# Kernel optimization log

Hardware: AMD Instinct MI355X
Metric: run time of the kernel (lower is better)

The kernel has to match this reference:

```python
import jax, jax.numpy as jnp
import numpy as np

N_NODES = 500_000
N_EDGES = 8_000_000
IN_DIM, HID_DIM, OUT_DIM = 10, 35, 2


def setup_inputs() -> dict:
    key = jax.random.key(0)
    k1, k2, k3, k4 = jax.random.split(key, 4)
    x = jax.random.normal(k1, (N_NODES, IN_DIM), dtype=jnp.float32)
    edge_index = jax.random.randint(k2, (2, N_EDGES), 0, N_NODES, dtype=jnp.int64)
    # Glorot-style init for GCNConv weights
    W1 = jax.random.normal(k3, (IN_DIM, HID_DIM), dtype=jnp.float32) * (1.0 / np.sqrt(IN_DIM))
    b1 = jnp.zeros((HID_DIM,), dtype=jnp.float32)
    W2 = jax.random.normal(k4, (HID_DIM, OUT_DIM), dtype=jnp.float32) * (1.0 / np.sqrt(HID_DIM))
    b2 = jnp.zeros((OUT_DIM,), dtype=jnp.float32)
    return {"x": x, "edge_index": edge_index, "W1": W1, "b1": b1, "W2": W2, "b2": b2}


def reference(x, edge_index, W1, b1, W2, b2):
    N = x.shape[0]
    # GCNConv: add self-loops, symmetric normalization D^-1/2 (A+I) D^-1/2
    loops = jnp.arange(N, dtype=edge_index.dtype)
    src = jnp.concatenate([edge_index[0], loops])  # [E+N]
    dst = jnp.concatenate([edge_index[1], loops])  # [E+N]
    deg = jax.ops.segment_sum(jnp.ones(src.shape, dtype=x.dtype), dst, num_segments=N)
    dinv = jax.lax.rsqrt(jnp.maximum(deg, 1.0))  # deg >= 1 due to self-loops
    norm = dinv[src] * dinv[dst]  # [E+N]

    def conv(h, W, b):
        h = h @ W                                  # [N, d_out] dense transform
        msg = h[src] * norm[:, None]               # gather + per-edge scale
        return jax.ops.segment_sum(msg, dst, num_segments=N) + b  # scatter-add

    h = jax.nn.relu(conv(x, W1, b1))
    # F.dropout(training=False) is identity in eval mode
    h = conv(h, W2, b2)
    return jax.nn.log_softmax(h, axis=1)
```

## Files before the change

kernel.cpp:

```cpp
#include <hip/hip_runtime.h>
#include <math.h>

constexpr int N_NODES = 500000;
constexpr int N_EDGES = 8000000;
constexpr int IN_DIM = 10, HID_DIM = 35, OUT_DIM = 2;

constexpr int BUCKET_BITS = 11;
constexpr int BNODES = 1 << BUCKET_BITS;
constexpr int NB = (N_NODES + BNODES - 1) / BNODES;
constexpr int NBP = 256;

constexpr int PART_TPB = 1024;
constexpr int EPT = 16;
constexpr int TILE = PART_TPB * EPT;
constexpr int NTILES = (N_EDGES + TILE - 1) / TILE;

__global__ void zero_small_kernel(unsigned* __restrict__ bcount) {
    bcount[threadIdx.x] = 0u;
}

__global__ void hist_kernel(const int* __restrict__ dst, unsigned* __restrict__ bcount, int E) {
    __shared__ unsigned h[NBP];
    h[threadIdx.x] = 0u;
    __syncthreads();
    int stride = gridDim.x * blockDim.x;
    for (int e = blockIdx.x * blockDim.x + threadIdx.x; e < E; e += stride)
        atomicAdd(&h[dst[e] >> BUCKET_BITS], 1u);
    __syncthreads();
    if (h[threadIdx.x]) atomicAdd(&bcount[threadIdx.x], h[threadIdx.x]);
}

__global__ void scan_kernel(const unsigned* __restrict__ bcount,
                            unsigned* __restrict__ bbase, unsigned* __restrict__ bcursor,
                            unsigned* __restrict__ rowstart) {
    __shared__ unsigned s[NBP];
    int t = threadIdx.x;
    unsigned v = bcount[t];
    s[t] = v; __syncthreads();
    for (int off = 1; off < NBP; off <<= 1) {
        unsigned a = (t >= off) ? s[t - off] : 0u;
        __syncthreads();
        s[t] += a;
        __syncthreads();
    }
    bbase[t] = s[t] - v;  bcursor[t] = s[t] - v;
    if (t == 0) { bbase[NBP] = (unsigned)N_EDGES; rowstart[N_NODES] = (unsigned)N_EDGES; }
}

__global__ __launch_bounds__(PART_TPB) void partition_kernel(
        const int* __restrict__ src, const int* __restrict__ dst,
        unsigned* __restrict__ bcursor, unsigned* __restrict__ packed, int E) {
    __shared__ unsigned h[NBP], base[NBP], c2[NBP];
    int t = threadIdx.x;
    for (int k = t; k < NBP; k += PART_TPB) { h[k] = 0u; c2[k] = 0u; }
    __syncthreads();
    int tile0 = blockIdx.x * TILE;
    int d[EPT];
    #pragma unroll
    for (int q = 0; q < EPT; ++q) {
        int e = tile0 + q * PART_TPB + t;
        d[q] = (e < E) ? dst[e] : -1;
        if (d[q] >= 0) atomicAdd(&h[d[q] >> BUCKET_BITS], 1u);
    }
    __syncthreads();
    for (int k = t; k < NBP; k += PART_TPB)
        if (h[k]) base[k] = atomicAdd(&bcursor[k], h[k]);
    __syncthreads();
    #pragma unroll
    for (int q = 0; q < EPT; ++q) {
        int e = tile0 + q * PART_TPB + t;
        if (d[q] >= 0) {
            int b = d[q] >> BUCKET_BITS;
            unsigned pos = base[b] + atomicAdd(&c2[b], 1u);
            packed[pos] = ((unsigned)src[e] << BUCKET_BITS) | (unsigned)(d[q] & (BNODES - 1));
        }
    }
}

__global__ __launch_bounds__(1024) void csrbuild_kernel(
        const unsigned* __restrict__ packed, const unsigned* __restrict__ bbase,
        unsigned* __restrict__ rowstart, int* __restrict__ csr,
        float* __restrict__ dinv, float* __restrict__ x, int N) {
    __shared__ unsigned cnt[BNODES];
    __shared__ unsigned pref[BNODES];
    __shared__ unsigned stmp[1024];
    int b = blockIdx.x, t = threadIdx.x;
    cnt[t] = 0u; cnt[t + 1024] = 0u;
    __syncthreads();
    unsigned base = bbase[b], end = bbase[b + 1];
    for (unsigned e = base + t; e < end; e += 1024)
        atomicAdd(&cnt[packed[e] & (BNODES - 1)], 1u);
    __syncthreads();
    unsigned a0 = cnt[2 * t], a1 = cnt[2 * t + 1];
    unsigned tsum = a0 + a1;
    stmp[t] = tsum; __syncthreads();
    for (int off = 1; off < 1024; off <<= 1) {
        unsigned a = (t >= off) ? stmp[t - off] : 0u;
        __syncthreads();
        stmp[t] += a;
        __syncthreads();
    }
    unsigned pre = stmp[t] - tsum;
    pref[2 * t] = pre; pref[2 * t + 1] = pre + a0;
    __syncthreads();
    int node0 = b << BUCKET_BITS;
    for (int k = t; k < BNODES; k += 1024) {
        int i = node0 + k;
        if (i < N) {
            rowstart[i] = base + pref[k];
            float di = rsqrtf((float)cnt[k] + 1.0f);
            dinv[i] = di;
            float2* xr = reinterpret_cast<float2*>(x + (size_t)i * IN_DIM);
            #pragma unroll
            for (int q = 0; q < 5; ++q) { float2 v = xr[q]; v.x *= di; v.y *= di; xr[q] = v; }
        }
    }
    __syncthreads();
    for (unsigned e = base + t; e < end; e += 1024) {
        unsigned p = packed[e];
        unsigned dl = p & (BNODES - 1);
        unsigned pos = base + atomicAdd(&pref[dl], 1u);
        csr[pos] = (int)(p >> BUCKET_BITS);
    }
}

__global__ __launch_bounds__(256) void gather1_kernel(
        const int* __restrict__ csr, const unsigned* __restrict__ rowstart,
        const float* __restrict__ xs, const float* __restrict__ dinv,
        const float* __restrict__ W1, const float* __restrict__ b1,
        const float* __restrict__ W2, float2* __restrict__ ts, int N) {
    __shared__ float sW1[IN_DIM * HID_DIM];
    __shared__ float sb1[HID_DIM];
    __shared__ float sW2[HID_DIM * OUT_DIM];
    for (int k = threadIdx.x; k < IN_DIM * HID_DIM; k += 256) sW1[k] = W1[k];
    if (threadIdx.x < HID_DIM) sb1[threadIdx.x] = b1[threadIdx.x];
    if (threadIdx.x < HID_DIM * OUT_DIM) sW2[threadIdx.x] = W2[threadIdx.x];
    __syncthreads();

    int i = blockIdx.x * 256 + threadIdx.x;
    if (i >= N) return;
    unsigned beg = rowstart[i], end = rowstart[i + 1];
    float v[IN_DIM];
    const float2* xi = reinterpret_cast<const float2*>(xs + (size_t)i * IN_DIM);
    #pragma unroll
    for (int q = 0; q < 5; ++q) { float2 u = xi[q]; v[2*q] = u.x; v[2*q+1] = u.y; }
    unsigned e = beg;
    int s = (e < end) ? csr[e] : 0;
    while (e < end) {
        int sn = (e + 1 < end) ? csr[e + 1] : 0;
        const float2* xr = reinterpret_cast<const float2*>(xs + (size_t)s * IN_DIM);
        #pragma unroll
        for (int q = 0; q < 5; ++q) { float2 u = xr[q]; v[2*q] += u.x; v[2*q+1] += u.y; }
        s = sn; ++e;
    }
    float di = dinv[i];
    #pragma unroll
    for (int k = 0; k < IN_DIM; ++k) v[k] *= di;
    float t0 = 0.0f, t1 = 0.0f;
    #pragma unroll
    for (int j = 0; j < HID_DIM; ++j) {
        float hh = sb1[j];
        #pragma unroll
        for (int q = 0; q < IN_DIM; ++q) hh = fmaf(v[q], sW1[q * HID_DIM + j], hh);
        hh = fmaxf(hh, 0.0f);
        t0 = fmaf(hh, sW2[2*j+0], t0);
        t1 = fmaf(hh, sW2[2*j+1], t1);
    }
    ts[i] = make_float2(t0 * di, t1 * di);
}

__global__ __launch_bounds__(256) void gather2_kernel(
        const int* __restrict__ csr, const unsigned* __restrict__ rowstart,
        const float2* __restrict__ ts, const float* __restrict__ dinv,
        const float* __restrict__ b2, float2* __restrict__ out, int N) {
    int i = blockIdx.x * 256 + threadIdx.x;
    if (i >= N) return;
    unsigned beg = rowstart[i], end = rowstart[i + 1];
    float2 acc = ts[i];
    unsigned e = beg;
    int s = (e < end) ? csr[e] : 0;
    while (e < end) {
        int sn = (e + 1 < end) ? csr[e + 1] : 0;
        float2 tv = ts[s];
        acc.x += tv.x; acc.y += tv.y;
        s = sn; ++e;
    }
    float di = dinv[i];
    float a0 = di * acc.x + b2[0];
    float a1 = di * acc.y + b2[1];
    float m = fmaxf(a0, a1);
    float lse = m + logf(expf(a0 - m) + expf(a1 - m));
    out[i] = make_float2(a0 - lse, a1 - lse);
}

extern "C" void kernel_launch(void* const* d_in, const int* in_sizes, int n_in,
                              void* d_out, int out_size, void* d_ws, size_t ws_size,
                              hipStream_t stream) {
    float* x        = (float*)d_in[0];
    const int* ei   = (const int*)d_in[1];
    const float* W1 = (const float*)d_in[2];
    const float* b1 = (const float*)d_in[3];
    const float* W2 = (const float*)d_in[4];
    const float* b2 = (const float*)d_in[5];
    float2* out = (float2*)d_out;

    const int* src = ei;
    const int* dst = ei + N_EDGES;

    unsigned* bcount   = (unsigned*)d_ws;
    unsigned* bbase    = bcount + NBP;
    unsigned* bcursor  = bbase + NBP + 1;
    unsigned* rowstart = bcursor + NBP;
    float*    dinv     = (float*)(rowstart + N_NODES + 1);
    float2*   ts       = (float2*)(dinv + N_NODES);
    unsigned* packed   = (unsigned*)(ts + N_NODES);
    int*      csr      = (int*)(packed + N_EDGES);

    const int node_grid = (N_NODES + 255) / 256;

    zero_small_kernel<<<1, NBP, 0, stream>>>(bcount);
    hist_kernel<<<1024, NBP, 0, stream>>>(dst, bcount, N_EDGES);
    scan_kernel<<<1, NBP, 0, stream>>>(bcount, bbase, bcursor, rowstart);
    partition_kernel<<<NTILES, PART_TPB, 0, stream>>>(src, dst, bcursor, packed, N_EDGES);
    csrbuild_kernel<<<NB, 1024, 0, stream>>>(packed, bbase, rowstart, csr, dinv, x, N_NODES);
    gather1_kernel<<<node_grid, 256, 0, stream>>>(csr, rowstart, x, dinv, W1, b1, W2, ts, N_NODES);
    gather2_kernel<<<node_grid, 256, 0, stream>>>(csr, rowstart, ts, dinv, b2, out, N_NODES);
}
```

Measured before the change: 650.9 us.

## Sort CSR neighbors by source chunk and sweep chunks in lockstep in gather1

The CSR build now bins each edge by destination node and by a 32K-node source chunk, so every row lists its neighbors grouped by chunk in increasing order. gather1 walks the chunks in a shared outer loop, so the threads of a block tend to read from the same region of x at the same time. The intent is better L2 locality for the random x gathers. It also moves gather1 to 1024-thread blocks with an occupancy hint, and adds a 32K-entry shared histogram plus extra branching per edge.

Measured after the change: 659.4 us. About the same (+1.3%).

```diff
diff --git a/kernel.cpp b/kernel.cpp
--- a/kernel.cpp
+++ b/kernel.cpp
@@ -9,6 +9,10 @@
 constexpr int BNODES = 1 << BUCKET_BITS;
 constexpr int NB = (N_NODES + BNODES - 1) / BNODES;
 constexpr int NBP = 256;
+
+constexpr int CHUNK_SHIFT = 15;
+constexpr int NCHUNK = 16;
+constexpr int NBIN2 = BNODES * NCHUNK;
 
 constexpr int PART_TPB = 1024;
 constexpr int EPT = 16;
@@ -81,18 +85,26 @@
         const unsigned* __restrict__ packed, const unsigned* __restrict__ bbase,
         unsigned* __restrict__ rowstart, int* __restrict__ csr,
         float* __restrict__ dinv, float* __restrict__ x, int N) {
-    __shared__ unsigned cnt[BNODES];
-    __shared__ unsigned pref[BNODES];
+    __shared__ unsigned cnt2[NBIN2];
     __shared__ unsigned stmp[1024];
     int b = blockIdx.x, t = threadIdx.x;
-    cnt[t] = 0u; cnt[t + 1024] = 0u;
+    #pragma unroll
+    for (int k = 0; k < NBIN2 / 1024; ++k) cnt2[t + k * 1024] = 0u;
     __syncthreads();
     unsigned base = bbase[b], end = bbase[b + 1];
-    for (unsigned e = base + t; e < end; e += 1024)
-        atomicAdd(&cnt[packed[e] & (BNODES - 1)], 1u);
-    __syncthreads();
-    unsigned a0 = cnt[2 * t], a1 = cnt[2 * t + 1];
-    unsigned tsum = a0 + a1;
+    for (unsigned e = base + t; e < end; e += 1024) {
+        unsigned p = packed[e];
+        unsigned bin = ((p & (BNODES - 1)) << 4) | (p >> (BUCKET_BITS + CHUNK_SHIFT));
+        atomicAdd(&cnt2[bin], 1u);
+    }
+    __syncthreads();
+    unsigned loc[32];
+    unsigned deg0 = 0, deg1 = 0;
+    #pragma unroll
+    for (int k = 0; k < 16; ++k) { loc[k] = cnt2[32 * t + k]; deg0 += loc[k]; }
+    #pragma unroll
+    for (int k = 16; k < 32; ++k) { loc[k] = cnt2[32 * t + k]; deg1 += loc[k]; }
+    unsigned tsum = deg0 + deg1;
     stmp[t] = tsum; __syncthreads();
     for (int off = 1; off < 1024; off <<= 1) {
         unsigned a = (t >= off) ? stmp[t - off] : 0u;
@@ -100,31 +112,37 @@
         stmp[t] += a;
         __syncthreads();
     }
-    unsigned pre = stmp[t] - tsum;
-    pref[2 * t] = pre; pref[2 * t + 1] = pre + a0;
-    __syncthreads();
+    unsigned run = stmp[t] - tsum;
+    #pragma unroll
+    for (int k = 0; k < 32; ++k) { cnt2[32 * t + k] = run; run += loc[k]; }
     int node0 = b << BUCKET_BITS;
-    for (int k = t; k < BNODES; k += 1024) {
-        int i = node0 + k;
-        if (i < N) {
-            rowstart[i] = base + pref[k];
-            float di = rsqrtf((float)cnt[k] + 1.0f);
-            dinv[i] = di;
-            float2* xr = reinterpret_cast<float2*>(x + (size_t)i * IN_DIM);
-            #pragma unroll
-            for (int q = 0; q < 5; ++q) { float2 v = xr[q]; v.x *= di; v.y *= di; xr[q] = v; }
-        }
+    int i0 = node0 + 2 * t, i1 = i0 + 1;
+    if (i0 < N) {
+        rowstart[i0] = base + cnt2[32 * t];
+        float di = rsqrtf((float)deg0 + 1.0f);
+        dinv[i0] = di;
+        float2* xr = reinterpret_cast<float2*>(x + (size_t)i0 * IN_DIM);
+        #pragma unroll
+        for (int q = 0; q < 5; ++q) { float2 v = xr[q]; v.x *= di; v.y *= di; xr[q] = v; }
+    }
+    if (i1 < N) {
+        rowstart[i1] = base + cnt2[32 * t + 16];
+        float di = rsqrtf((float)deg1 + 1.0f);
+        dinv[i1] = di;
+        float2* xr = reinterpret_cast<float2*>(x + (size_t)i1 * IN_DIM);
+        #pragma unroll
+        for (int q = 0; q < 5; ++q) { float2 v = xr[q]; v.x *= di; v.y *= di; xr[q] = v; }
     }
     __syncthreads();
     for (unsigned e = base + t; e < end; e += 1024) {
         unsigned p = packed[e];
-        unsigned dl = p & (BNODES - 1);
-        unsigned pos = base + atomicAdd(&pref[dl], 1u);
+        unsigned bin = ((p & (BNODES - 1)) << 4) | (p >> (BUCKET_BITS + CHUNK_SHIFT));
+        unsigned pos = base + atomicAdd(&cnt2[bin], 1u);
         csr[pos] = (int)(p >> BUCKET_BITS);
     }
 }
 
-__global__ __launch_bounds__(256) void gather1_kernel(
+__global__ __launch_bounds__(1024, 8) void gather1_kernel(
         const int* __restrict__ csr, const unsigned* __restrict__ rowstart,
         const float* __restrict__ xs, const float* __restrict__ dinv,
         const float* __restrict__ W1, const float* __restrict__ b1,
@@ -132,26 +150,29 @@
     __shared__ float sW1[IN_DIM * HID_DIM];
     __shared__ float sb1[HID_DIM];
     __shared__ float sW2[HID_DIM * OUT_DIM];
-    for (int k = threadIdx.x; k < IN_DIM * HID_DIM; k += 256) sW1[k] = W1[k];
-    if (threadIdx.x < HID_DIM) sb1[threadIdx.x] = b1[threadIdx.x];
-    if (threadIdx.x < HID_DIM * OUT_DIM) sW2[threadIdx.x] = W2[threadIdx.x];
-    __syncthreads();
-
-    int i = blockIdx.x * 256 + threadIdx.x;
+    int t = threadIdx.x;
+    for (int k = t; k < IN_DIM * HID_DIM; k += 1024) sW1[k] = W1[k];
+    if (t < HID_DIM) sb1[t] = b1[t];
+    if (t < HID_DIM * OUT_DIM) sW2[t] = W2[t];
+    __syncthreads();
+
+    int i = blockIdx.x * 1024 + t;
     if (i >= N) return;
-    unsigned beg = rowstart[i], end = rowstart[i + 1];
+    unsigned ptr = rowstart[i], end = rowstart[i + 1];
     float v[IN_DIM];
     const float2* xi = reinterpret_cast<const float2*>(xs + (size_t)i * IN_DIM);
     #pragma unroll
     for (int q = 0; q < 5; ++q) { float2 u = xi[q]; v[2*q] = u.x; v[2*q+1] = u.y; }
-    unsigned e = beg;
-    int s = (e < end) ? csr[e] : 0;
-    while (e < end) {
-        int sn = (e + 1 < end) ? csr[e + 1] : 0;
-        const float2* xr = reinterpret_cast<const float2*>(xs + (size_t)s * IN_DIM);
-        #pragma unroll
-        for (int q = 0; q < 5; ++q) { float2 u = xr[q]; v[2*q] += u.x; v[2*q+1] += u.y; }
-        s = sn; ++e;
+    #pragma unroll 1
+    for (int c = 0; c < NCHUNK; ++c) {
+        while (ptr < end) {
+            int s = csr[ptr];
+            if ((s >> CHUNK_SHIFT) != c) break;
+            const float2* xr = reinterpret_cast<const float2*>(xs + (size_t)s * IN_DIM);
+            #pragma unroll
+            for (int q = 0; q < 5; ++q) { float2 u = xr[q]; v[2*q] += u.x; v[2*q+1] += u.y; }
+            ++ptr;
+        }
     }
     float di = dinv[i];
     #pragma unroll
@@ -216,13 +237,11 @@
     unsigned* packed   = (unsigned*)(ts + N_NODES);
     int*      csr      = (int*)(packed + N_EDGES);
 
-    const int node_grid = (N_NODES + 255) / 256;
-
     zero_small_kernel<<<1, NBP, 0, stream>>>(bcount);
     hist_kernel<<<1024, NBP, 0, stream>>>(dst, bcount, N_EDGES);
     scan_kernel<<<1, NBP, 0, stream>>>(bcount, bbase, bcursor, rowstart);
     partition_kernel<<<NTILES, PART_TPB, 0, stream>>>(src, dst, bcursor, packed, N_EDGES);
     csrbuild_kernel<<<NB, 1024, 0, stream>>>(packed, bbase, rowstart, csr, dinv, x, N_NODES);
-    gather1_kernel<<<node_grid, 256, 0, stream>>>(csr, rowstart, x, dinv, W1, b1, W2, ts, N_NODES);
-    gather2_kernel<<<node_grid, 256, 0, stream>>>(csr, rowstart, ts, dinv, b2, out, N_NODES);
-}
+    gather1_kernel<<<(N_NODES + 1023) / 1024, 1024, 0, stream>>>(csr, rowstart, x, dinv, W1, b1, W2, ts, N_NODES);
+    gather2_kernel<<<(N_NODES + 255) / 256, 256, 0, stream>>>(csr, rowstart, ts, dinv, b2, out, N_NODES);
+}
```

## Pad scaled features to 64-byte rows, vectorize histogram, unroll gather loops

Applied to the files above, without the earlier changes.

Adds a padx kernel that writes dinv-scaled features into a 16-float-per-row buffer that reuses the packed workspace. This lets gather1 load each neighbour row with aligned float4 loads and touch one cache line per row. It also stops csrbuild from scaling the input x in place. The histogram now reads dst as int4, both gather loops are unrolled by two to keep more loads in flight, and gather1 uses 1024-thread blocks. The cost is an extra kernel launch plus an extra pass over the features, and the padded buffer is larger than the original rows.

Measured after the change: 571.0 us. 1.14x faster.

```diff
diff --git a/kernel.cpp b/kernel.cpp
--- a/kernel.cpp
+++ b/kernel.cpp
@@ -19,13 +19,19 @@
     bcount[threadIdx.x] = 0u;
 }
 
-__global__ void hist_kernel(const int* __restrict__ dst, unsigned* __restrict__ bcount, int E) {
+__global__ void hist_kernel(const int4* __restrict__ dst4, unsigned* __restrict__ bcount,
+                            int E4) {
     __shared__ unsigned h[NBP];
     h[threadIdx.x] = 0u;
     __syncthreads();
     int stride = gridDim.x * blockDim.x;
-    for (int e = blockIdx.x * blockDim.x + threadIdx.x; e < E; e += stride)
-        atomicAdd(&h[dst[e] >> BUCKET_BITS], 1u);
+    for (int e = blockIdx.x * blockDim.x + threadIdx.x; e < E4; e += stride) {
+        int4 v = dst4[e];
+        atomicAdd(&h[v.x >> BUCKET_BITS], 1u);
+        atomicAdd(&h[v.y >> BUCKET_BITS], 1u);
+        atomicAdd(&h[v.z >> BUCKET_BITS], 1u);
+        atomicAdd(&h[v.w >> BUCKET_BITS], 1u);
+    }
     __syncthreads();
     if (h[threadIdx.x]) atomicAdd(&bcount[threadIdx.x], h[threadIdx.x]);
 }
@@ -80,7 +86,7 @@
 __global__ __launch_bounds__(1024) void csrbuild_kernel(
         const unsigned* __restrict__ packed, const unsigned* __restrict__ bbase,
         unsigned* __restrict__ rowstart, int* __restrict__ csr,
-        float* __restrict__ dinv, float* __restrict__ x, int N) {
+        float* __restrict__ dinv, int N) {
     __shared__ unsigned cnt[BNODES];
     __shared__ unsigned pref[BNODES];
     __shared__ unsigned stmp[1024];
@@ -108,11 +114,7 @@
         int i = node0 + k;
         if (i < N) {
             rowstart[i] = base + pref[k];
-            float di = rsqrtf((float)cnt[k] + 1.0f);
-            dinv[i] = di;
-            float2* xr = reinterpret_cast<float2*>(x + (size_t)i * IN_DIM);
-            #pragma unroll
-            for (int q = 0; q < 5; ++q) { float2 v = xr[q]; v.x *= di; v.y *= di; xr[q] = v; }
+            dinv[i] = rsqrtf((float)cnt[k] + 1.0f);
         }
     }
     __syncthreads();
@@ -124,34 +126,67 @@
     }
 }
 
-__global__ __launch_bounds__(256) void gather1_kernel(
+__global__ void padx_kernel(const float* __restrict__ x, const float* __restrict__ dinv,
+                            float* __restrict__ xp, int N) {
+    int i = blockIdx.x * 256 + threadIdx.x;
+    if (i >= N) return;
+    float di = dinv[i];
+    const float2* xr = reinterpret_cast<const float2*>(x + (size_t)i * IN_DIM);
+    float2 t0 = xr[0], t1 = xr[1], t2 = xr[2], t3 = xr[3], t4 = xr[4];
+    float4* op = reinterpret_cast<float4*>(xp + ((size_t)i << 4));
+    op[0] = make_float4(t0.x * di, t0.y * di, t1.x * di, t1.y * di);
+    op[1] = make_float4(t2.x * di, t2.y * di, t3.x * di, t3.y * di);
+    op[2] = make_float4(t4.x * di, t4.y * di, 0.0f, 0.0f);
+    op[3] = make_float4(0.0f, 0.0f, 0.0f, 0.0f);
+}
+
+__global__ __launch_bounds__(1024) void gather1_kernel(
         const int* __restrict__ csr, const unsigned* __restrict__ rowstart,
-        const float* __restrict__ xs, const float* __restrict__ dinv,
+        const float* __restrict__ xp, const float* __restrict__ dinv,
         const float* __restrict__ W1, const float* __restrict__ b1,
         const float* __restrict__ W2, float2* __restrict__ ts, int N) {
     __shared__ float sW1[IN_DIM * HID_DIM];
     __shared__ float sb1[HID_DIM];
     __shared__ float sW2[HID_DIM * OUT_DIM];
-    for (int k = threadIdx.x; k < IN_DIM * HID_DIM; k += 256) sW1[k] = W1[k];
-    if (threadIdx.x < HID_DIM) sb1[threadIdx.x] = b1[threadIdx.x];
-    if (threadIdx.x < HID_DIM * OUT_DIM) sW2[threadIdx.x] = W2[threadIdx.x];
-    __syncthreads();
-
-    int i = blockIdx.x * 256 + threadIdx.x;
+    int t = threadIdx.x;
+    for (int k = t; k < IN_DIM * HID_DIM; k += 1024) sW1[k] = W1[k];
+    if (t < HID_DIM) sb1[t] = b1[t];
+    if (t < HID_DIM * OUT_DIM) sW2[t] = W2[t];
+    __syncthreads();
+
+    int i = blockIdx.x * 1024 + t;
     if (i >= N) return;
-    unsigned beg = rowstart[i], end = rowstart[i + 1];
+    unsigned e = rowstart[i], end = rowstart[i + 1];
     float v[IN_DIM];
-    const float2* xi = reinterpret_cast<const float2*>(xs + (size_t)i * IN_DIM);
-    #pragma unroll
-    for (int q = 0; q < 5; ++q) { float2 u = xi[q]; v[2*q] = u.x; v[2*q+1] = u.y; }
-    unsigned e = beg;
-    int s = (e < end) ? csr[e] : 0;
-    while (e < end) {
-        int sn = (e + 1 < end) ? csr[e + 1] : 0;
-        const float2* xr = reinterpret_cast<const float2*>(xs + (size_t)s * IN_DIM);
-        #pragma unroll
-        for (int q = 0; q < 5; ++q) { float2 u = xr[q]; v[2*q] += u.x; v[2*q+1] += u.y; }
-        s = sn; ++e;
+    {
+        const float4* xi = reinterpret_cast<const float4*>(xp + ((size_t)i << 4));
+        float4 a = xi[0], b = xi[1];
+        float2 c = reinterpret_cast<const float2*>(xi)[4];
+        v[0] = a.x; v[1] = a.y; v[2] = a.z; v[3] = a.w;
+        v[4] = b.x; v[5] = b.y; v[6] = b.z; v[7] = b.w;
+        v[8] = c.x; v[9] = c.y;
+    }
+    while (e + 1 < end) {
+        int s0 = csr[e], s1 = csr[e + 1];
+        const float4* r0 = reinterpret_cast<const float4*>(xp + ((size_t)s0 << 4));
+        const float4* r1 = reinterpret_cast<const float4*>(xp + ((size_t)s1 << 4));
+        float4 a0 = r0[0], q0 = r0[1];
+        float2 c0 = reinterpret_cast<const float2*>(r0)[4];
+        float4 a1 = r1[0], q1 = r1[1];
+        float2 c1 = reinterpret_cast<const float2*>(r1)[4];
+        v[0] += a0.x + a1.x; v[1] += a0.y + a1.y; v[2] += a0.z + a1.z; v[3] += a0.w + a1.w;
+        v[4] += q0.x + q1.x; v[5] += q0.y + q1.y; v[6] += q0.z + q1.z; v[7] += q0.w + q1.w;
+        v[8] += c0.x + c1.x; v[9] += c0.y + c1.y;
+        e += 2;
+    }
+    if (e < end) {
+        int s = csr[e];
+        const float4* r = reinterpret_cast<const float4*>(xp + ((size_t)s << 4));
+        float4 a = r[0], q = r[1];
+        float2 c = reinterpret_cast<const float2*>(r)[4];
+        v[0] += a.x; v[1] += a.y; v[2] += a.z; v[3] += a.w;
+        v[4] += q.x; v[5] += q.y; v[6] += q.z; v[7] += q.w;
+        v[8] += c.x; v[9] += c.y;
     }
     float di = dinv[i];
     #pragma unroll
@@ -163,8 +198,8 @@
         #pragma unroll
         for (int q = 0; q < IN_DIM; ++q) hh = fmaf(v[q], sW1[q * HID_DIM + j], hh);
         hh = fmaxf(hh, 0.0f);
-        t0 = fmaf(hh, sW2[2*j+0], t0);
-        t1 = fmaf(hh, sW2[2*j+1], t1);
+        t0 = fmaf(hh, sW2[2 * j + 0], t0);
+        t1 = fmaf(hh, sW2[2 * j + 1], t1);
     }
     ts[i] = make_float2(t0 * di, t1 * di);
 }
@@ -175,15 +210,17 @@
         const float* __restrict__ b2, float2* __restrict__ out, int N) {
     int i = blockIdx.x * 256 + threadIdx.x;
     if (i >= N) return;
-    unsigned beg = rowstart[i], end = rowstart[i + 1];
+    unsigned e = rowstart[i], end = rowstart[i + 1];
     float2 acc = ts[i];
-    unsigned e = beg;
-    int s = (e < end) ? csr[e] : 0;
-    while (e < end) {
-        int sn = (e + 1 < end) ? csr[e + 1] : 0;
-        float2 tv = ts[s];
+    while (e + 1 < end) {
+        int s0 = csr[e], s1 = csr[e + 1];
+        float2 t0 = ts[s0], t1 = ts[s1];
+        acc.x += t0.x + t1.x; acc.y += t0.y + t1.y;
+        e += 2;
+    }
+    if (e < end) {
+        float2 tv = ts[csr[e]];
         acc.x += tv.x; acc.y += tv.y;
-        s = sn; ++e;
     }
     float di = dinv[i];
     float a0 = di * acc.x + b2[0];
@@ -196,8 +233,8 @@
 extern "C" void kernel_launch(void* const* d_in, const int* in_sizes, int n_in,
                               void* d_out, int out_size, void* d_ws, size_t ws_size,
                               hipStream_t stream) {
-    float* x        = (float*)d_in[0];
-    const int* ei   = (const int*)d_in[1];
+    const float* x  = (const float*)d_in[0];
+    const int*   ei = (const int*)d_in[1];
     const float* W1 = (const float*)d_in[2];
     const float* b1 = (const float*)d_in[3];
     const float* W2 = (const float*)d_in[4];
@@ -215,14 +252,14 @@
     float2*   ts       = (float2*)(dinv + N_NODES);
     unsigned* packed   = (unsigned*)(ts + N_NODES);
     int*      csr      = (int*)(packed + N_EDGES);
-
-    const int node_grid = (N_NODES + 255) / 256;
+    float*    xp       = (float*)packed;
 
     zero_small_kernel<<<1, NBP, 0, stream>>>(bcount);
-    hist_kernel<<<1024, NBP, 0, stream>>>(dst, bcount, N_EDGES);
+    hist_kernel<<<1024, NBP, 0, stream>>>((const int4*)dst, bcount, N_EDGES / 4);
     scan_kernel<<<1, NBP, 0, stream>>>(bcount, bbase, bcursor, rowstart);
     partition_kernel<<<NTILES, PART_TPB, 0, stream>>>(src, dst, bcursor, packed, N_EDGES);
-    csrbuild_kernel<<<NB, 1024, 0, stream>>>(packed, bbase, rowstart, csr, dinv, x, N_NODES);
-    gather1_kernel<<<node_grid, 256, 0, stream>>>(csr, rowstart, x, dinv, W1, b1, W2, ts, N_NODES);
-    gather2_kernel<<<node_grid, 256, 0, stream>>>(csr, rowstart, ts, dinv, b2, out, N_NODES);
-}
+    csrbuild_kernel<<<NB, 1024, 0, stream>>>(packed, bbase, rowstart, csr, dinv, N_NODES);
+    padx_kernel<<<(N_NODES + 255) / 256, 256, 0, stream>>>(x, dinv, xp, N_NODES);
+    gather1_kernel<<<(N_NODES + 1023) / 1024, 1024, 0, stream>>>(csr, rowstart, xp, dinv, W1, b1, W2, ts, N_NODES);
+    gather2_kernel<<<(N_NODES + 255) / 256, 256, 0, stream>>>(csr, rowstart, ts, dinv, b2, out, N_NODES);
+}
```
